# Optimization experiments

Measured on AMD Instinct MI355X. Metric: run time of the kernel, lower is better.

Reference implementation:

```python
import jax, jax.numpy as jnp
import numpy as np

TOP_K = 4
ALPHA = 1.702
LIMIT = 7.0


def setup_inputs() -> dict:
    key = jax.random.key(0)
    ks = jax.random.split(key, 7)
    B, S, H, I, E = 1, 512, 2880, 2880, 16
    s = 0.02
    return {
        "hidden_states": jax.random.normal(ks[0], (B, S, H), dtype=jnp.float32),
        "router_w": jax.random.normal(ks[1], (H, E), dtype=jnp.float32) * s,
        "router_b": jax.random.normal(ks[2], (E,), dtype=jnp.float32) * s,
        "gate_up_w": jax.random.normal(ks[3], (E, H, 2 * I), dtype=jnp.float32) * s,
        "gate_up_b": jax.random.normal(ks[4], (E, 2 * I), dtype=jnp.float32) * s,
        "down_w": jax.random.normal(ks[5], (E, I, H), dtype=jnp.float32) * s,
        "down_b": jax.random.normal(ks[6], (E, H), dtype=jnp.float32) * s,
    }


def reference(hidden_states, router_w, router_b, gate_up_w, gate_up_b, down_w, down_b):
    B, S, H = hidden_states.shape
    x = hidden_states.reshape(-1, H)                      # [T, H]
    T = x.shape[0]

    # Router: top-k + softmax over selected logits, scattered back to [T, E]
    router_logits = x @ router_w + router_b               # [T, E]
    top_v, top_i = jax.lax.top_k(router_logits, TOP_K)    # [T, K]
    top_v = jax.nn.softmax(top_v, axis=-1)
    router_scores = jnp.zeros_like(router_logits).at[
        jnp.arange(T)[:, None], top_i
    ].set(top_v)                                          # [T, E]

    # Dense all-experts GLU (matches the repeat-across-experts formulation)
    gate_up = jnp.einsum('th,ehd->etd', x, gate_up_w) + gate_up_b[:, None, :]  # [E, T, 2I]
    gate = gate_up[..., ::2]                              # [E, T, I]
    up = gate_up[..., 1::2]                               # [E, T, I]
    gate = jnp.minimum(gate, LIMIT)
    up = jnp.clip(up, -LIMIT, LIMIT)
    glu = gate * jax.nn.sigmoid(gate * ALPHA)
    expert_out = jnp.einsum('eti,eih->eth', (up + 1.0) * glu, down_w) + down_b[:, None, :]  # [E, T, H]

    # Masked combine with routing weights
    out = jnp.sum(expert_out * router_scores.T[:, :, None], axis=0)  # [T, H]
    return (out.reshape(B, S, H),)
```

## Files before the change

### kernel.cpp

```cpp
#include <hip/hip_runtime.h>
#include <hip/hip_bf16.h>

#define NTOK 512
#define HDIM 2880
#define NGU  5760
#define NEXP 16
#define KSTEPS 90
#define KSH   45
#define MT 160
#define MFR 10
#define NPAIR (NTOK*4)
#define PARTELT ((size_t)NPAIR * HDIM)

typedef float  f32x4  __attribute__((ext_vector_type(4)));
typedef float  f32x2  __attribute__((ext_vector_type(2)));
typedef short  bf16x8 __attribute__((ext_vector_type(8)));

__device__ __forceinline__ unsigned short f2bf(float f) {
  union { float f; unsigned u; } a; a.f = f;
  unsigned r = a.u + 0x7FFFu + ((a.u >> 16) & 1u);
  return (unsigned short)(r >> 16);
}
__device__ __forceinline__ float bflo(unsigned u) {
  union { unsigned u; float f; } c; c.u = u << 16; return c.f;
}
__device__ __forceinline__ float bfhi(unsigned u) {
  union { unsigned u; float f; } c; c.u = u & 0xffff0000u; return c.f;
}

__device__ __forceinline__ void lds_barrier() {
  asm volatile("s_waitcnt lgkmcnt(0)" ::: "memory");
  __builtin_amdgcn_s_barrier();
  asm volatile("" ::: "memory");
}


__global__ __launch_bounds__(256) void k_router(
    const float* __restrict__ x, const float* __restrict__ rw,
    const float* __restrict__ rb, int* __restrict__ counts,
    int* __restrict__ top_e, float* __restrict__ top_w,
    unsigned short* __restrict__ xb)
{
  const int t = blockIdx.x;
  const int tid = threadIdx.x;
  __shared__ float red[256][17];
  float acc[NEXP];
#pragma unroll
  for (int e = 0; e < NEXP; ++e) acc[e] = 0.f;
  const float* xr = x + (size_t)t * HDIM;
  unsigned short* xbr = xb + (size_t)t * HDIM;
  for (int h = tid; h < HDIM; h += 256) {
    float xv = xr[h];
    xbr[h] = f2bf(xv);
    const f32x4* wr = (const f32x4*)(rw + (size_t)h * NEXP);
#pragma unroll
    for (int q = 0; q < 4; ++q) {
      f32x4 w = wr[q];
#pragma unroll
      for (int j = 0; j < 4; ++j) acc[q*4+j] += xv * w[j];
    }
  }
#pragma unroll
  for (int e = 0; e < NEXP; ++e) red[tid][e] = acc[e];
  __syncthreads();
  for (int s = 128; s > 0; s >>= 1) {
    if (tid < s) {
#pragma unroll
      for (int e = 0; e < NEXP; ++e) red[tid][e] += red[tid + s][e];
    }
    __syncthreads();
  }
  if (tid == 0) {
    float v[NEXP];
#pragma unroll
    for (int e = 0; e < NEXP; ++e) v[e] = red[0][e] + rb[e];
    int mask = 0; float tv[4]; int ti[4];
    for (int k = 0; k < 4; ++k) {
      float best = -3.4e38f; int bi = 0;
      for (int e = 0; e < NEXP; ++e)
        if (!((mask >> e) & 1) && v[e] > best) { best = v[e]; bi = e; }
      mask |= 1 << bi; tv[k] = best; ti[k] = bi;
    }
    float s = 0.f, ex[4];
    for (int k = 0; k < 4; ++k) { ex[k] = __expf(tv[k] - tv[0]); s += ex[k]; }
    float inv = 1.f / s;
    for (int k = 0; k < 4; ++k) {
      top_e[t*4+k] = ti[k];
      top_w[t*4+k] = ex[k] * inv;
      atomicAdd(&counts[ti[k]], 1);
    }
  }
}

__global__ __launch_bounds__(64) void k_fill(
    const int* __restrict__ top_e, const float* __restrict__ top_w,
    const int* __restrict__ counts, int* __restrict__ seg,
    int* __restrict__ pair_tok, float* __restrict__ pair_w,
    int* __restrict__ pair_of)
{
  const int e = blockIdx.x;
  const int lane = threadIdx.x;
  int base = 0;
  for (int i = 0; i < e; ++i) base += counts[i];
  if (lane == 0) {
    seg[e] = base;
    if (e == NEXP - 1) seg[NEXP] = base + counts[e];
  }
  for (int t0 = 0; t0 < NTOK; t0 += 64) {
    int t = t0 + lane;
    int my = -1;
#pragma unroll
    for (int k = 0; k < 4; ++k) if (top_e[t*4+k] == e) my = k;
    unsigned long long m = __ballot(my >= 0);
    if (my >= 0) {
      int pre = __popcll(m & ((1ull << lane) - 1ull));
      pair_tok[base + pre] = t;
      pair_w[base + pre] = top_w[t*4+my];
      pair_of[t*4 + my] = base + pre;
    }
    base += (int)__popcll(m);
  }
}

__global__ __launch_bounds__(256, 2) void k_gateup(
    const unsigned short* __restrict__ xb, const float* __restrict__ gw,
    const float* __restrict__ gb, const int* __restrict__ seg,
    const int* __restrict__ pair_tok, const float* __restrict__ pair_w,
    unsigned short* __restrict__ act)
{
  const int e = blockIdx.z;
  const int segs = seg[e];
  const int n_e = seg[e+1] - segs;
  const int m0 = blockIdx.y * MT;
  if (m0 >= n_e) return;
  const int tid = threadIdx.x;
  const int lane = tid & 63;
  const int wid = tid >> 6;
  const int l15 = lane & 15, lg = lane >> 4;
  const int fcb = blockIdx.x * 128 + wid * 32;
  const int fcE = fcb + 2*l15;
  const int colf = min(2*fcb + 4*l15, NGU - 4);

  __shared__ unsigned short Alds[2][MT][40];

  const float* Bq = gw + (size_t)e * HDIM * NGU + colf + (size_t)lg * 8 * NGU;

  const unsigned short* sp0 = nullptr;
  const unsigned short* sp1 = nullptr;
  const int r0 = tid >> 1, h0 = tid & 1;
  const int r1 = (tid + 256) >> 1, h1 = tid & 1;
  if (m0 + r0 < n_e) sp0 = xb + (size_t)pair_tok[segs + m0 + r0] * HDIM + h0*16;
  if (tid < 2*MT - 256 && m0 + r1 < n_e)
    sp1 = xb + (size_t)pair_tok[segs + m0 + r1] * HDIM + h1*16;

  f32x4 accgE[MFR], accuE[MFR], accgO[MFR], accuO[MFR];
  {
    f32x4 b = __builtin_nontemporal_load((const f32x4*)(gb + (size_t)e * NGU + colf));
#pragma unroll
    for (int m = 0; m < MFR; ++m)
#pragma unroll
      for (int r = 0; r < 4; ++r) {
        accgE[m][r] = b[0]; accuE[m][r] = b[1];
        accgO[m][r] = b[2]; accuO[m][r] = b[3];
      }
  }

  auto stage = [&](int ks, int b) {
    bf16x8 z = {0,0,0,0,0,0,0,0};
    bf16x8 v0 = z, v1 = z;
    if (sp0) { v0 = *(const bf16x8*)(sp0 + ks*32); v1 = *(const bf16x8*)(sp0 + ks*32 + 8); }
    *(bf16x8*)&Alds[b][r0][h0*16]     = v0;
    *(bf16x8*)&Alds[b][r0][h0*16 + 8] = v1;
    if (tid < 2*MT - 256) {
      bf16x8 w0 = z, w1 = z;
      if (sp1) { w0 = *(const bf16x8*)(sp1 + ks*32); w1 = *(const bf16x8*)(sp1 + ks*32 + 8); }
      *(bf16x8*)&Alds[b][r1][h1*16]     = w0;
      *(bf16x8*)&Alds[b][r1][h1*16 + 8] = w1;
    }
  };

  f32x4 bA[8];
  auto loadB = [&](int ks) {
    const float* bp = Bq + (size_t)ks * 32 * NGU;
#pragma unroll
    for (int j = 0; j < 8; ++j)
      bA[j] = __builtin_nontemporal_load((const f32x4*)(bp + (size_t)j * NGU));
  };

  loadB(0);
  stage(0, 0);
  lds_barrier();
  int buf = 0;

  for (int ks = 0; ks < KSTEPS; ++ks) {
    if (ks + 1 < KSTEPS) stage(ks + 1, buf ^ 1);
    bf16x8 bgE, buE, bgO, buO;
#pragma unroll
    for (int j = 0; j < 8; ++j) {
      bgE[j] = (short)f2bf(bA[j][0]); buE[j] = (short)f2bf(bA[j][1]);
      bgO[j] = (short)f2bf(bA[j][2]); buO[j] = (short)f2bf(bA[j][3]);
    }
    if (ks + 1 < KSTEPS) loadB(ks + 1);
#pragma unroll
    for (int m = 0; m < MFR; ++m) {
      bf16x8 a = *(const bf16x8*)&Alds[buf][m*16 + l15][lg*8];
      accgE[m] = __builtin_amdgcn_mfma_f32_16x16x32_bf16(a, bgE, accgE[m], 0, 0, 0);
      accuE[m] = __builtin_amdgcn_mfma_f32_16x16x32_bf16(a, buE, accuE[m], 0, 0, 0);
      accgO[m] = __builtin_amdgcn_mfma_f32_16x16x32_bf16(a, bgO, accgO[m], 0, 0, 0);
      accuO[m] = __builtin_amdgcn_mfma_f32_16x16x32_bf16(a, buO, accuO[m], 0, 0, 0);
    }
    lds_barrier();
    buf ^= 1;
  }

  if (fcE < HDIM) {
#pragma unroll
    for (int m = 0; m < MFR; ++m) {
#pragma unroll
      for (int r = 0; r < 4; ++r) {
        int grow = m0 + m*16 + lg*4 + r;
        if (grow < n_e) {
          float pw = pair_w[segs + grow];
          float gE = fminf(accgE[m][r], 7.f);
          float uE = fminf(fmaxf(accuE[m][r], -7.f), 7.f);
          float avE = (uE + 1.f) * (gE / (1.f + __expf(-1.702f * gE))) * pw;
          float gO = fminf(accgO[m][r], 7.f);
          float uO = fminf(fmaxf(accuO[m][r], -7.f), 7.f);
          float avO = (uO + 1.f) * (gO / (1.f + __expf(-1.702f * gO))) * pw;
          unsigned pk = (unsigned)f2bf(avE) | ((unsigned)f2bf(avO) << 16);
          *(unsigned*)&act[(size_t)(segs + grow) * HDIM + fcE] = pk;
        }
      }
    }
  }
}

__global__ __launch_bounds__(256, 3) void k_down(
    const unsigned short* __restrict__ act, const float* __restrict__ dw,
    const int* __restrict__ seg, const int* __restrict__ pair_tok,
    unsigned short* __restrict__ partial)
{
  const int e = blockIdx.z;
  const int mi = blockIdx.y >> 1;
  const int kh = blockIdx.y & 1;
  const int segs = seg[e];
  const int n_e = seg[e+1] - segs;
  const int m0 = mi * MT;
  if (m0 >= n_e) return;
  const int tid = threadIdx.x;
  const int lane = tid & 63;
  const int wid = tid >> 6;
  const int l15 = lane & 15, lg = lane >> 4;
  const int cb = blockIdx.x * 128 + wid * 32;
  const int cE = cb + 2*l15;
  const int colc = min(cE, HDIM - 2);
  const int k0 = kh * (KSH * 32);

  __shared__ unsigned short Alds[2][MT][40];

  unsigned short* po = partial + (size_t)kh * PARTELT;
  const float* Bq = dw + (size_t)e * HDIM * HDIM + colc
                  + (size_t)(k0 + lg * 8) * HDIM;

  const unsigned short* sp0 = nullptr;
  const unsigned short* sp1 = nullptr;
  const int r0 = tid >> 1, h0 = tid & 1;
  const int r1 = (tid + 256) >> 1, h1 = tid & 1;
  if (m0 + r0 < n_e) sp0 = act + (size_t)(segs + m0 + r0) * HDIM + k0 + h0*16;
  if (tid < 2*MT - 256 && m0 + r1 < n_e)
    sp1 = act + (size_t)(segs + m0 + r1) * HDIM + k0 + h1*16;

  f32x4 accE[MFR], accO[MFR];
#pragma unroll
  for (int m = 0; m < MFR; ++m)
#pragma unroll
    for (int r = 0; r < 4; ++r) { accE[m][r] = 0.f; accO[m][r] = 0.f; }

  auto stage = [&](int ks, int b) {
    bf16x8 z = {0,0,0,0,0,0,0,0};
    bf16x8 v0 = z, v1 = z;
    if (sp0) { v0 = *(const bf16x8*)(sp0 + ks*32); v1 = *(const bf16x8*)(sp0 + ks*32 + 8); }
    *(bf16x8*)&Alds[b][r0][h0*16]     = v0;
    *(bf16x8*)&Alds[b][r0][h0*16 + 8] = v1;
    if (tid < 2*MT - 256) {
      bf16x8 w0 = z, w1 = z;
      if (sp1) { w0 = *(const bf16x8*)(sp1 + ks*32); w1 = *(const bf16x8*)(sp1 + ks*32 + 8); }
      *(bf16x8*)&Alds[b][r1][h1*16]     = w0;
      *(bf16x8*)&Alds[b][r1][h1*16 + 8] = w1;
    }
  };

  f32x2 bA[8];
  auto loadB = [&](int ks) {
    const float* bp = Bq + (size_t)ks * 32 * HDIM;
#pragma unroll
    for (int j = 0; j < 8; ++j)
      bA[j] = __builtin_nontemporal_load((const f32x2*)(bp + (size_t)j * HDIM));
  };

  loadB(0);
  stage(0, 0);
  lds_barrier();
  int buf = 0;

  for (int ks = 0; ks < KSH; ++ks) {
    if (ks + 1 < KSH) stage(ks + 1, buf ^ 1);
    bf16x8 bfE, bfO;
#pragma unroll
    for (int j = 0; j < 8; ++j) { bfE[j] = (short)f2bf(bA[j][0]); bfO[j] = (short)f2bf(bA[j][1]); }
    if (ks + 1 < KSH) loadB(ks + 1);
#pragma unroll
    for (int m = 0; m < MFR; ++m) {
      bf16x8 a = *(const bf16x8*)&Alds[buf][m*16 + l15][lg*8];
      accE[m] = __builtin_amdgcn_mfma_f32_16x16x32_bf16(a, bfE, accE[m], 0, 0, 0);
      accO[m] = __builtin_amdgcn_mfma_f32_16x16x32_bf16(a, bfO, accO[m], 0, 0, 0);
    }
    lds_barrier();
    buf ^= 1;
  }

  if (cE < HDIM) {
#pragma unroll
    for (int m = 0; m < MFR; ++m) {
#pragma unroll
      for (int r = 0; r < 4; ++r) {
        int grow = m0 + m*16 + lg*4 + r;
        if (grow < n_e) {
          unsigned pk = (unsigned)f2bf(accE[m][r]) | ((unsigned)f2bf(accO[m][r]) << 16);
          *(unsigned*)&po[(size_t)(segs + grow) * HDIM + cE] = pk;
        }
      }
    }
  }
}

__global__ __launch_bounds__(256) void k_gather(
    const unsigned short* __restrict__ partial, const int* __restrict__ pair_of,
    const int* __restrict__ top_e, const float* __restrict__ top_w,
    const float* __restrict__ db, float* __restrict__ out)
{
  const int t = blockIdx.x;
  const int tid = threadIdx.x;
  const int p0 = pair_of[t*4+0], p1 = pair_of[t*4+1];
  const int p2 = pair_of[t*4+2], p3 = pair_of[t*4+3];
  const float w0 = top_w[t*4+0], w1 = top_w[t*4+1];
  const float w2 = top_w[t*4+2], w3 = top_w[t*4+3];
  const unsigned short* r[8] = {
    partial + (size_t)p0 * HDIM,           partial + (size_t)p1 * HDIM,
    partial + (size_t)p2 * HDIM,           partial + (size_t)p3 * HDIM,
    partial + PARTELT + (size_t)p0 * HDIM, partial + PARTELT + (size_t)p1 * HDIM,
    partial + PARTELT + (size_t)p2 * HDIM, partial + PARTELT + (size_t)p3 * HDIM };
  const float* b0 = db + (size_t)top_e[t*4+0] * HDIM;
  const float* b1 = db + (size_t)top_e[t*4+1] * HDIM;
  const float* b2 = db + (size_t)top_e[t*4+2] * HDIM;
  const float* b3 = db + (size_t)top_e[t*4+3] * HDIM;
  float* o = out + (size_t)t * HDIM;
  for (int p = tid; p < HDIM/4; p += 256) {
    f32x4 s;
    {
      f32x4 c0 = *(const f32x4*)(b0 + 4*p);
      f32x4 c1 = *(const f32x4*)(b1 + 4*p);
      f32x4 c2 = *(const f32x4*)(b2 + 4*p);
      f32x4 c3 = *(const f32x4*)(b3 + 4*p);
#pragma unroll
      for (int j = 0; j < 4; ++j)
        s[j] = (w0*c0[j] + w1*c1[j]) + (w2*c2[j] + w3*c3[j]);
    }
#pragma unroll
    for (int q = 0; q < 8; ++q) {
      uint2 v = *(const uint2*)(r[q] + 4*p);
      s[0] += bflo(v.x); s[1] += bfhi(v.x);
      s[2] += bflo(v.y); s[3] += bfhi(v.y);
    }
    *(f32x4*)(o + 4*p) = s;
  }
}


extern "C" void kernel_launch(void* const* d_in, const int* in_sizes, int n_in,
                              void* d_out, int out_size, void* d_ws, size_t ws_size,
                              hipStream_t stream) {
  const float* x  = (const float*)d_in[0];
  const float* rw = (const float*)d_in[1];
  const float* rb = (const float*)d_in[2];
  const float* gw = (const float*)d_in[3];
  const float* gb = (const float*)d_in[4];
  const float* dw = (const float*)d_in[5];
  const float* db = (const float*)d_in[6];
  float* out = (float*)d_out;

  char* w = (char*)d_ws;
  int*   counts   = (int*)(w);
  int*   seg      = (int*)(w + 64);
  int*   top_e    = (int*)(w + 1024);
  float* top_w    = (float*)(w + 1024 + 8192);
  int*   pair_tok = (int*)(w + 1024 + 16384);
  float* pair_w   = (float*)(w + 1024 + 24576);
  int*   pair_of  = (int*)(w + 1024 + 32768);
  unsigned short* xb  = (unsigned short*)(w + (1 << 20));
  unsigned short* act = (unsigned short*)(w + (8 << 20));
  unsigned short* partial = (unsigned short*)(w + (24ull << 20));

  hipMemsetAsync(counts, 0, NEXP * sizeof(int), stream);
  k_router<<<NTOK, 256, 0, stream>>>(x, rw, rb, counts, top_e, top_w, xb);
  k_fill<<<NEXP, 64, 0, stream>>>(top_e, top_w, counts, seg, pair_tok, pair_w, pair_of);

  dim3 gg(23, 2, NEXP);
  k_gateup<<<gg, 256, 0, stream>>>(xb, gw, gb, seg, pair_tok, pair_w, act);

  dim3 gd(23, 4, NEXP);
  k_down<<<gd, 256, 0, stream>>>(act, dw, seg, pair_tok, partial);

  k_gather<<<NTOK, 256, 0, stream>>>(partial, pair_of, top_e, top_w, db, out);
}
```

Baseline: 428.9 us.

## Stage gate_up weight tile through LDS with coalesced row loads

Each thread used to load its own strided 8-row column slice of the fp32 gate_up weights directly into registers. Now the block cooperatively loads the 32x256 weight tile with row-contiguous float4 loads, converts it to bf16 once, and writes it to a double-buffered LDS tile that the MFMA loop then reads back. The intent is better global coalescing and no duplicated conversion. The cost is extra LDS traffic and capacity, possible bank conflicts on the strided ushort4 reads, and lower occupancy.

```diff
diff --git a/kernel.cpp b/kernel.cpp
--- a/kernel.cpp
+++ b/kernel.cpp
@@ -140,10 +140,16 @@
   const int fcb = blockIdx.x * 128 + wid * 32;
   const int fcE = fcb + 2*l15;
   const int colf = min(2*fcb + 4*l15, NGU - 4);
+  const int cloc = wid*64 + 4*l15;
 
   __shared__ unsigned short Alds[2][MT][40];
-
-  const float* Bq = gw + (size_t)e * HDIM * NGU + colf + (size_t)lg * 8 * NGU;
+  __shared__ unsigned short Blds[2][32][256];
+
+  const float* We = gw + (size_t)e * HDIM * NGU;
+  const int colbase = blockIdx.x * 256;
+  const int srow = tid >> 6;
+  const int scol = (tid & 63) * 4;
+  const int gcol = min(colbase + scol, NGU - 4);
 
   const unsigned short* sp0 = nullptr;
   const unsigned short* sp1 = nullptr;
@@ -179,28 +185,42 @@
     }
   };
 
-  f32x4 bA[8];
-  auto loadB = [&](int ks) {
-    const float* bp = Bq + (size_t)ks * 32 * NGU;
-#pragma unroll
-    for (int j = 0; j < 8; ++j)
-      bA[j] = __builtin_nontemporal_load((const f32x4*)(bp + (size_t)j * NGU));
+  f32x4 sreg[8];
+  auto loadBq = [&](int ks) {
+#pragma unroll
+    for (int q = 0; q < 8; ++q) {
+      const float* p = We + (size_t)(ks*32 + q*4 + srow) * NGU + gcol;
+      sreg[q] = __builtin_nontemporal_load((const f32x4*)p);
+    }
   };
-
-  loadB(0);
+  auto writeB = [&](int b) {
+#pragma unroll
+    for (int q = 0; q < 8; ++q) {
+      ushort4 o;
+      o.x = f2bf(sreg[q][0]); o.y = f2bf(sreg[q][1]);
+      o.z = f2bf(sreg[q][2]); o.w = f2bf(sreg[q][3]);
+      *(ushort4*)&Blds[b][q*4 + srow][scol] = o;
+    }
+  };
+
+  loadBq(0);
   stage(0, 0);
+  writeB(0);
   lds_barrier();
   int buf = 0;
 
   for (int ks = 0; ks < KSTEPS; ++ks) {
-    if (ks + 1 < KSTEPS) stage(ks + 1, buf ^ 1);
+    if (ks + 1 < KSTEPS) { loadBq(ks + 1); stage(ks + 1, buf ^ 1); }
+    ushort4 v[8];
+#pragma unroll
+    for (int j = 0; j < 8; ++j)
+      v[j] = *(const ushort4*)&Blds[buf][lg*8 + j][cloc];
     bf16x8 bgE, buE, bgO, buO;
 #pragma unroll
     for (int j = 0; j < 8; ++j) {
-      bgE[j] = (short)f2bf(bA[j][0]); buE[j] = (short)f2bf(bA[j][1]);
-      bgO[j] = (short)f2bf(bA[j][2]); buO[j] = (short)f2bf(bA[j][3]);
-    }
-    if (ks + 1 < KSTEPS) loadB(ks + 1);
+      bgE[j] = (short)v[j].x; buE[j] = (short)v[j].y;
+      bgO[j] = (short)v[j].z; buO[j] = (short)v[j].w;
+    }
 #pragma unroll
     for (int m = 0; m < MFR; ++m) {
       bf16x8 a = *(const bf16x8*)&Alds[buf][m*16 + l15][lg*8];
@@ -209,6 +229,7 @@
       accgO[m] = __builtin_amdgcn_mfma_f32_16x16x32_bf16(a, bgO, accgO[m], 0, 0, 0);
       accuO[m] = __builtin_amdgcn_mfma_f32_16x16x32_bf16(a, buO, accuO[m], 0, 0, 0);
     }
+    if (ks + 1 < KSTEPS) writeB(buf ^ 1);
     lds_barrier();
     buf ^= 1;
   }
```

After: 481.6 us. 1.12x slower.
